# Optimization experiments

Measured on AMD Instinct MI355X. Metric: run time of the kernel, lower is better.

## Reference

```python
import jax, jax.numpy as jnp
import numpy as np

GROUP_SIZES = (64, 128, 256, 96, 160, 224, 192, 288, 320, 112, 80, 48, 32, 16, 32)
LENGTH = 512
ALPHABET = 21


def setup_inputs() -> dict:
    key = jax.random.key(0)
    keys = jax.random.split(key, len(GROUP_SIZES) + 1)
    n_samples = int(sum(GROUP_SIZES))
    inp = {"x": jax.random.normal(keys[0], (n_samples, LENGTH, ALPHABET), dtype=jnp.float32)}
    for i, g in enumerate(GROUP_SIZES):
        inp[f"mat{i}"] = jax.random.normal(keys[i + 1], (g, g), dtype=jnp.float32)
    return inp


def reference(x, mat0, mat1, mat2, mat3, mat4, mat5, mat6, mat7, mat8, mat9,
              mat10, mat11, mat12, mat13, mat14):
    mats = (mat0, mat1, mat2, mat3, mat4, mat5, mat6, mat7, mat8, mat9,
            mat10, mat11, mat12, mat13, mat14)
    # Block-diagonal grouped matmul along the sample dim: out[sl] = mats_i @ x[sl].
    # Group boundaries are static Python ints, so slicing is jit-friendly.
    pieces = []
    start = 0
    for m, g in zip(mats, GROUP_SIZES):
        xg = x[start:start + g]  # (g, L, A)
        pieces.append(jnp.einsum('gh,hla->gla', m, xg))
        start += g
    return jnp.concatenate(pieces, axis=0)
```

## Files before the change

kernel.cpp:

```cpp
#include <hip/hip_runtime.h>
#include <hip/hip_bf16.h>

#define NCOL 10752
#define NROW 2048
#define NG 15
#define NTILES 23

typedef __bf16 bf16;
typedef __attribute__((ext_vector_type(8))) __bf16 bf16x8;
typedef __attribute__((ext_vector_type(4))) __bf16 bf16x4;
typedef __attribute__((ext_vector_type(4))) float f32x4;

__constant__ int c_gsize[NG]  = {64,128,256,96,160,224,192,288,320,112,80,48,32,16,32};
__constant__ int c_gstart[NG] = {0,64,192,448,544,704,928,1120,1408,1728,1840,1920,1968,2000,2016};
__constant__ int c_tgrp[NTILES] = {0,1,2,2,3,4,4,5,5,6,6,7,7,7,8,8,8,9,10,11,12,13,14};
__constant__ int c_trow[NTILES] = {0,0,0,128,0,0,128,0,128,0,128,0,128,256,0,128,256,0,0,0,0,0,0};

struct MatPtrs { const float* p[NG]; };

constexpr int BM = 128, BN = 128, BK = 32, BKp = 40;

__global__ __launch_bounds__(256)
void matapply_kernel(const float* __restrict__ x, MatPtrs mats, float* __restrict__ out)
{
    __shared__ bf16 sA[BM][BKp];
    __shared__ bf16 sB[BN][BKp];

    const int tid    = threadIdx.x;
    const int tileid = blockIdx.x;
    const int colb   = blockIdx.y * BN;

    const int grp  = c_tgrp[tileid];
    const int row0 = c_trow[tileid];
    const int g    = c_gsize[grp];
    const int s    = c_gstart[grp];
    const float* __restrict__ M = mats.p[grp];

    const int wave = tid >> 6;
    const int lane = tid & 63;
    const int wr   = (wave & 1) * 64;
    const int wc   = (wave >> 1) * 64;
    const int lm   = lane & 15;
    const int kq   = lane >> 4;
    const int kb   = kq * 8;

    const int aK = (tid & 7) * 4;
    const int aR = tid >> 3;
    const int bC = (tid & 31) * 4;
    const int bK = (tid >> 5) * 4;

    f32x4 acc[4][4];
    #pragma unroll
    for (int i = 0; i < 4; i++)
        #pragma unroll
        for (int j = 0; j < 4; j++)
            acc[i][j] = (f32x4){0.f, 0.f, 0.f, 0.f};

    for (int k0 = 0; k0 < g; k0 += BK) {
        #pragma unroll
        for (int i = 0; i < 4; i++) {
            int r = aR + 32 * i;
            float4 v = make_float4(0.f, 0.f, 0.f, 0.f);
            if ((row0 + r) < g && (k0 + aK) < g)
                v = *(const float4*)(M + (size_t)(row0 + r) * g + (k0 + aK));
            bf16x4 w;
            w[0] = (bf16)v.x; w[1] = (bf16)v.y; w[2] = (bf16)v.z; w[3] = (bf16)v.w;
            *(bf16x4*)&sA[r][aK] = w;
        }

        float4 xv[4];
        #pragma unroll
        for (int j = 0; j < 4; j++)
            xv[j] = *(const float4*)(x + (size_t)(s + k0 + bK + j) * NCOL + colb + bC);
        #pragma unroll
        for (int cc = 0; cc < 4; cc++) {
            int lc = bC + cc;
            bf16x4 w;
            #pragma unroll
            for (int j = 0; j < 4; j++)
                w[j] = (bf16)(((const float*)&xv[j])[cc]);
            *(bf16x4*)&sB[lc][bK ^ (((lc >> 2) & 3) << 3)] = w;
        }

        __syncthreads();

        bf16x8 af[4], bfr[4];
        #pragma unroll
        for (int i = 0; i < 4; i++)
            af[i] = *(const bf16x8*)&sA[wr + i * 16 + lm][kb];
        #pragma unroll
        for (int j = 0; j < 4; j++) {
            int lc = wc + j * 16 + lm;
            bfr[j] = *(const bf16x8*)&sB[lc][kb ^ (((lc >> 2) & 3) << 3)];
        }
        #pragma unroll
        for (int i = 0; i < 4; i++)
            #pragma unroll
            for (int j = 0; j < 4; j++)
                acc[i][j] = __builtin_amdgcn_mfma_f32_16x16x32_bf16(af[i], bfr[j], acc[i][j], 0, 0, 0);

        __syncthreads();
    }

    #pragma unroll
    for (int i = 0; i < 4; i++) {
        #pragma unroll
        for (int r = 0; r < 4; r++) {
            int row = row0 + wr + i * 16 + kq * 4 + r;
            if (row < g) {
                float* orow = out + (size_t)(s + row) * NCOL + colb + wc;
                #pragma unroll
                for (int j = 0; j < 4; j++)
                    orow[j * 16 + lm] = acc[i][j][r];
            }
        }
    }
}

extern "C" void kernel_launch(void* const* d_in, const int* in_sizes, int n_in,
                              void* d_out, int out_size, void* d_ws, size_t ws_size,
                              hipStream_t stream)
{
    const float* x = (const float*)d_in[0];
    MatPtrs mp;
    for (int i = 0; i < NG; i++) mp.p[i] = (const float*)d_in[1 + i];
    float* out = (float*)d_out;

    dim3 grid(NTILES, NCOL / BN);
    dim3 block(256);
    matapply_kernel<<<grid, block, 0, stream>>>(x, mp, out);
}
```

Measured before the change: 209.1 us.

## Double-buffer LDS tiles with register prefetch and schedule largest groups first

Shared-memory A/B tiles become double-buffered. The next K-slice's global loads are issued into registers before the current MFMA block and written to the alternate buffer afterwards, which removes one barrier per iteration and overlaps memory latency with compute. The tile-to-group table is also reordered so the largest groups (longest K loops) are dispatched first, which should reduce tail imbalance. The cost is doubled LDS use and extra live registers, which may lower occupancy.

```diff
diff --git a/kernel.cpp b/kernel.cpp
--- a/kernel.cpp
+++ b/kernel.cpp
@@ -13,8 +13,8 @@
 
 __constant__ int c_gsize[NG]  = {64,128,256,96,160,224,192,288,320,112,80,48,32,16,32};
 __constant__ int c_gstart[NG] = {0,64,192,448,544,704,928,1120,1408,1728,1840,1920,1968,2000,2016};
-__constant__ int c_tgrp[NTILES] = {0,1,2,2,3,4,4,5,5,6,6,7,7,7,8,8,8,9,10,11,12,13,14};
-__constant__ int c_trow[NTILES] = {0,0,0,128,0,0,128,0,128,0,128,0,128,256,0,128,256,0,0,0,0,0,0};
+__constant__ int c_tgrp[NTILES] = {8,8,8,7,7,7,2,2,5,5,6,6,4,4,1,9,3,10,0,11,12,14,13};
+__constant__ int c_trow[NTILES] = {0,128,256,0,128,256,0,128,0,128,0,128,0,128,0,0,0,0,0,0,0,0,0};
 
 struct MatPtrs { const float* p[NG]; };
 
@@ -23,8 +23,8 @@
 __global__ __launch_bounds__(256)
 void matapply_kernel(const float* __restrict__ x, MatPtrs mats, float* __restrict__ out)
 {
-    __shared__ bf16 sA[BM][BKp];
-    __shared__ bf16 sB[BN][BKp];
+    __shared__ bf16 sA[2][BM][BKp];
+    __shared__ bf16 sB[2][BN][BKp];
 
     const int tid    = threadIdx.x;
     const int tileid = blockIdx.x;
@@ -49,6 +49,8 @@
     const int bC = (tid & 31) * 4;
     const int bK = (tid >> 5) * 4;
 
+    const int nIter = (g + BK - 1) / BK;
+
     f32x4 acc[4][4];
     #pragma unroll
     for (int i = 0; i < 4; i++)
@@ -56,42 +58,63 @@
         for (int j = 0; j < 4; j++)
             acc[i][j] = (f32x4){0.f, 0.f, 0.f, 0.f};
 
-    for (int k0 = 0; k0 < g; k0 += BK) {
-        #pragma unroll
-        for (int i = 0; i < 4; i++) {
-            int r = aR + 32 * i;
-            float4 v = make_float4(0.f, 0.f, 0.f, 0.f);
-            if ((row0 + r) < g && (k0 + aK) < g)
-                v = *(const float4*)(M + (size_t)(row0 + r) * g + (k0 + aK));
-            bf16x4 w;
-            w[0] = (bf16)v.x; w[1] = (bf16)v.y; w[2] = (bf16)v.z; w[3] = (bf16)v.w;
-            *(bf16x4*)&sA[r][aK] = w;
-        }
+    float4 av[4], xv[4];
 
-        float4 xv[4];
+    #pragma unroll
+    for (int i = 0; i < 4; i++) {
+        int r = aR + 32 * i;
+        av[i] = make_float4(0.f, 0.f, 0.f, 0.f);
+        if ((row0 + r) < g && aK < g)
+            av[i] = *(const float4*)(M + (size_t)(row0 + r) * g + aK);
+    }
+    #pragma unroll
+    for (int j = 0; j < 4; j++)
+        xv[j] = *(const float4*)(x + (size_t)(s + bK + j) * NCOL + colb + bC);
+
+    #pragma unroll
+    for (int i = 0; i < 4; i++) {
+        int r = aR + 32 * i;
+        bf16x4 w;
+        w[0] = (bf16)av[i].x; w[1] = (bf16)av[i].y; w[2] = (bf16)av[i].z; w[3] = (bf16)av[i].w;
+        *(bf16x4*)&sA[0][r][aK] = w;
+    }
+    #pragma unroll
+    for (int cc = 0; cc < 4; cc++) {
+        int lc = bC + cc;
+        bf16x4 w;
         #pragma unroll
         for (int j = 0; j < 4; j++)
-            xv[j] = *(const float4*)(x + (size_t)(s + k0 + bK + j) * NCOL + colb + bC);
-        #pragma unroll
-        for (int cc = 0; cc < 4; cc++) {
-            int lc = bC + cc;
-            bf16x4 w;
+            w[j] = (bf16)(((const float*)&xv[j])[cc]);
+        *(bf16x4*)&sB[0][lc][bK ^ (((lc >> 2) & 3) << 3)] = w;
+    }
+    __syncthreads();
+
+    for (int it = 0; it < nIter; ++it) {
+        const int cur = it & 1;
+        const bool more = (it + 1) < nIter;
+
+        if (more) {
+            const int k0 = (it + 1) * BK;
+            #pragma unroll
+            for (int i = 0; i < 4; i++) {
+                int r = aR + 32 * i;
+                av[i] = make_float4(0.f, 0.f, 0.f, 0.f);
+                if ((row0 + r) < g && (k0 + aK) < g)
+                    av[i] = *(const float4*)(M + (size_t)(row0 + r) * g + (k0 + aK));
+            }
             #pragma unroll
             for (int j = 0; j < 4; j++)
-                w[j] = (bf16)(((const float*)&xv[j])[cc]);
-            *(bf16x4*)&sB[lc][bK ^ (((lc >> 2) & 3) << 3)] = w;
+                xv[j] = *(const float4*)(x + (size_t)(s + k0 + bK + j) * NCOL + colb + bC);
         }
-
-        __syncthreads();
 
         bf16x8 af[4], bfr[4];
         #pragma unroll
         for (int i = 0; i < 4; i++)
-            af[i] = *(const bf16x8*)&sA[wr + i * 16 + lm][kb];
+            af[i] = *(const bf16x8*)&sA[cur][wr + i * 16 + lm][kb];
         #pragma unroll
         for (int j = 0; j < 4; j++) {
             int lc = wc + j * 16 + lm;
-            bfr[j] = *(const bf16x8*)&sB[lc][kb ^ (((lc >> 2) & 3) << 3)];
+            bfr[j] = *(const bf16x8*)&sB[cur][lc][kb ^ (((lc >> 2) & 3) << 3)];
         }
         #pragma unroll
         for (int i = 0; i < 4; i++)
@@ -99,7 +122,26 @@
             for (int j = 0; j < 4; j++)
                 acc[i][j] = __builtin_amdgcn_mfma_f32_16x16x32_bf16(af[i], bfr[j], acc[i][j], 0, 0, 0);
 
-        __syncthreads();
+        if (more) {
+            const int nxt = 1 - cur;
+            #pragma unroll
+            for (int i = 0; i < 4; i++) {
+                int r = aR + 32 * i;
+                bf16x4 w;
+                w[0] = (bf16)av[i].x; w[1] = (bf16)av[i].y; w[2] = (bf16)av[i].z; w[3] = (bf16)av[i].w;
+                *(bf16x4*)&sA[nxt][r][aK] = w;
+            }
+            #pragma unroll
+            for (int cc = 0; cc < 4; cc++) {
+                int lc = bC + cc;
+                bf16x4 w;
+                #pragma unroll
+                for (int j = 0; j < 4; j++)
+                    w[j] = (bf16)(((const float*)&xv[j])[cc]);
+                *(bf16x4*)&sB[nxt][lc][bK ^ (((lc >> 2) & 3) << 3)] = w;
+            }
+            __syncthreads();
+        }
     }
 
     #pragma unroll
```

Result: faster. 199.9 us (-4.4%).
